# Kernel tuning notes

Hardware: AMD Instinct MI355X
Metric: run time of the kernel (lower is better)

The kernel has to match this reference:

```python
import jax, jax.numpy as jnp
import numpy as np

LN_EPS = 1e-5

def _gelu(x):
    # matches the module's custom gelu: x * sigmoid(1.702 * x)
    return x * jax.nn.sigmoid(1.702 * x)

def setup_inputs() -> dict:
    key = jax.random.key(0)
    k1, k2, k3, k4 = jax.random.split(key, 4)
    B, d_in, d_out, E = 4096, 768, 1024, 10
    x = jax.random.normal(k1, (B, d_in), dtype=jnp.float32)
    x_cls_logits = jax.random.normal(k2, (B, E), dtype=jnp.float32)
    # expert weights (torch Linear stored transposed; here [in, out] acting as x @ W)
    W1 = jax.random.normal(k3, (E, d_in, d_out), dtype=jnp.float32) * (d_in ** -0.5)
    W2 = jax.random.normal(k4, (E, d_out, d_out), dtype=jnp.float32) * (d_out ** -0.5)
    ln_gamma = jnp.ones((E, d_out), dtype=jnp.float32)
    ln_beta = jnp.zeros((E, d_out), dtype=jnp.float32)
    return {"x": x, "x_cls_logits": x_cls_logits, "W1": W1, "W2": W2,
            "ln_gamma": ln_gamma, "ln_beta": ln_beta}

def reference(x, x_cls_logits, W1, W2, ln_gamma, ln_beta):
    B = x.shape[0]
    # top-1 routing: each sample goes to expert argmax(x_cls)
    cls = jnp.argmax(x_cls_logits, axis=1)                       # [B] int
    # compute all experts densely, then select per sample (grouped equivalent of
    # the per-sample Python-loop dispatch in the original forward)
    embed1_all = jnp.einsum('bi,eio->beo', x, W1)                # [B,E,d_out]
    embed2_all = jnp.einsum('beo,eop->bep', _gelu(embed1_all), W2)  # [B,E,d_out]
    s_all = embed1_all + embed2_all                              # [B,E,d_out]
    rows = jnp.arange(B)
    s = s_all[rows, cls]                                         # [B,d_out]
    # per-expert LayerNorm params gathered per sample
    g = ln_gamma[cls]                                            # [B,d_out]
    b = ln_beta[cls]                                             # [B,d_out]
    mean = jnp.mean(s, axis=-1, keepdims=True)
    var = jnp.mean(jnp.square(s - mean), axis=-1, keepdims=True)
    y = (s - mean) * jax.lax.rsqrt(var + LN_EPS) * g + b
    # L2 normalize embeddings
    out = y / jnp.linalg.norm(y, axis=-1, keepdims=True)
    return out, x_cls_logits
```

## Files before the change

### kernel.cpp

```cpp
#include <hip/hip_runtime.h>
#include <math.h>

#define BSAMP 4096
#define D_IN  768
#define D_OUT 1024
#define NEXP  10
#define LN_EPS 1e-5f
#define STEPS1 (D_IN / 64)
#define STEPS2 (D_OUT / 64)

#define NB_CVT1 (D_IN / 32 * 4 * NEXP)
#define NB_CVT2 (D_OUT / 32 * 4 * NEXP)
#define NB_XCVT (BSAMP * D_IN / 2048)
#define NB_PREP (1 + NB_CVT1 + NB_CVT2 + NB_XCVT)

typedef __attribute__((ext_vector_type(8))) short bf16x8;
typedef __attribute__((ext_vector_type(4))) float f32x4;

__device__ __forceinline__ float b2f(unsigned short u) {
    union { unsigned int i; float f; } v; v.i = ((unsigned int)u) << 16; return v.f;
}
__device__ __forceinline__ unsigned short f2b(float f) {
    union { float f; unsigned int i; } v; v.f = f;
    unsigned int x = v.i;
    unsigned int r = (x + 0x7fffu + ((x >> 16) & 1u)) >> 16;
    return (unsigned short)r;
}


__device__ __forceinline__ void cvt_body(const float* __restrict__ W,
                                         unsigned short* __restrict__ Wt,
                                         int K, int i, int tid) {
    const int KT = K >> 5;
    const int kt = i % KT;
    const int rest = i / KT;
    const int n = (rest & 3) * 256 + tid;
    const int e = rest >> 2;
    const float* src = W + ((size_t)e * K + (size_t)kt * 32) * D_OUT + n;
    unsigned short v[32];
    #pragma unroll
    for (int j = 0; j < 32; j++) v[j] = f2b(src[(size_t)j * D_OUT]);
    const int nt = n >> 7, nn = n & 127;
    unsigned short* dst = Wt + ((((size_t)e * 8 + nt) * KT + kt) << 12) + nn * 32;
    #pragma unroll
    for (int j = 0; j < 4; j++)
        *(bf16x8*)&dst[j * 8] = *(bf16x8*)&v[j * 8];
}

__global__ __launch_bounds__(256)
void k7_prep(const float* __restrict__ logits, const float* __restrict__ X,
             const float* __restrict__ W1, const float* __restrict__ W2,
             float* __restrict__ out1, int* __restrict__ cls,
             int* __restrict__ idx, int* __restrict__ offs,
             unsigned short* __restrict__ xb, unsigned short* __restrict__ W1t,
             unsigned short* __restrict__ W2t) {
    const int tid = threadIdx.x;
    const int blk = blockIdx.x;

    if (blk == 0) {
        __shared__ int cnt[NEXP];
        __shared__ int cur[NEXP];
        __shared__ int offsL[NEXP + 1];
        if (tid < NEXP) cnt[tid] = 0;
        __syncthreads();

        int be[16];
        #pragma unroll
        for (int j = 0; j < 16; j++) {
            int b = tid + 256 * j;
            const float* L = logits + (size_t)b * NEXP;
            float best = L[0]; int e0 = 0;
            #pragma unroll
            for (int e = 0; e < NEXP; e++) {
                float v = L[e];
                out1[(size_t)b * NEXP + e] = v;
                if (v > best) { best = v; e0 = e; }
            }
            be[j] = e0;
            cls[b] = e0;
            atomicAdd(&cnt[e0], 1);
        }
        __syncthreads();
        if (tid == 0) {
            int s = 0;
            for (int e = 0; e < NEXP; e++) { offsL[e] = s; cur[e] = s; s += cnt[e]; }
            offsL[NEXP] = s;
        }
        __syncthreads();
        if (tid <= NEXP) offs[tid] = offsL[tid];
        #pragma unroll
        for (int j = 0; j < 16; j++) {
            int b = tid + 256 * j;
            int p = atomicAdd(&cur[be[j]], 1);
            idx[p] = b;
        }
        return;
    }

    int i = blk - 1;
    if (i < NB_CVT1) { cvt_body(W1, W1t, D_IN, i, tid); return; }
    i -= NB_CVT1;
    if (i < NB_CVT2) { cvt_body(W2, W2t, D_OUT, i, tid); return; }
    i -= NB_CVT2;
    {
        int o = (i * 256 + tid) * 8;
        float4 v0 = *(const float4*)(X + o);
        float4 v1 = *(const float4*)(X + o + 4);
        unsigned short t[8] = { f2b(v0.x), f2b(v0.y), f2b(v0.z), f2b(v0.w),
                                f2b(v1.x), f2b(v1.y), f2b(v1.z), f2b(v1.w) };
        *(bf16x8*)(xb + o) = *(bf16x8*)t;
    }
}


#define GLDS(srcp, dstp) __builtin_amdgcn_global_load_lds( \
    (const __attribute__((address_space(1))) unsigned int*)(srcp), \
    (__attribute__((address_space(3))) unsigned int*)(dstp), 16, 0, 0)

#define STAGE_A(Ab, t) do { \
    _Pragma("unroll") \
    for (int j = 0; j < 2; j++) { \
        int c = tid + j * 256; \
        GLDS(aRow + (t) * 64 + (c >> 6) * 8, (Ab) + c * 8); \
    } \
} while (0)

#define STAGE_B(Bb, t) do { \
    _Pragma("unroll") \
    for (int j = 0; j < 4; j++) { \
        int c = tid + j * 256; \
        int kc = c >> 7; \
        GLDS(bPanel + ((size_t)(2 * (t) + (kc >> 2)) << 12) + (c & 127) * 32 + (kc & 3) * 8, \
             (Bb) + c * 8); \
    } \
} while (0)

#define COMPUTE(Ab, Bb) do { \
    _Pragma("unroll") \
    for (int s = 0; s < 2; s++) { \
        const unsigned short* ab_ = (Ab) + (s * 4 + quad) * 512; \
        const unsigned short* bb_ = (Bb) + (s * 4 + quad) * 1024; \
        bf16x8 a0 = *(const bf16x8*)&ab_[(wrow + l16) * 8]; \
        bf16x8 a1 = *(const bf16x8*)&ab_[(wrow + 16 + l16) * 8]; \
        bf16x8 b0 = *(const bf16x8*)&bb_[(wcol + l16) * 8]; \
        bf16x8 b1 = *(const bf16x8*)&bb_[(wcol + 16 + l16) * 8]; \
        bf16x8 b2 = *(const bf16x8*)&bb_[(wcol + 32 + l16) * 8]; \
        bf16x8 b3 = *(const bf16x8*)&bb_[(wcol + 48 + l16) * 8]; \
        acc[0][0] = __builtin_amdgcn_mfma_f32_16x16x32_bf16(a0, b0, acc[0][0], 0, 0, 0); \
        acc[0][1] = __builtin_amdgcn_mfma_f32_16x16x32_bf16(a0, b1, acc[0][1], 0, 0, 0); \
        acc[0][2] = __builtin_amdgcn_mfma_f32_16x16x32_bf16(a0, b2, acc[0][2], 0, 0, 0); \
        acc[0][3] = __builtin_amdgcn_mfma_f32_16x16x32_bf16(a0, b3, acc[0][3], 0, 0, 0); \
        acc[1][0] = __builtin_amdgcn_mfma_f32_16x16x32_bf16(a1, b0, acc[1][0], 0, 0, 0); \
        acc[1][1] = __builtin_amdgcn_mfma_f32_16x16x32_bf16(a1, b1, acc[1][1], 0, 0, 0); \
        acc[1][2] = __builtin_amdgcn_mfma_f32_16x16x32_bf16(a1, b2, acc[1][2], 0, 0, 0); \
        acc[1][3] = __builtin_amdgcn_mfma_f32_16x16x32_bf16(a1, b3, acc[1][3], 0, 0, 0); \
    } \
} while (0)

__global__ __launch_bounds__(256)
void k6_gemm1(const unsigned short* __restrict__ xb, const unsigned short* __restrict__ W1t,
              const int* __restrict__ offs, const int* __restrict__ idx,
              unsigned short* __restrict__ e1g, unsigned short* __restrict__ g1g) {
    const int e = blockIdx.z;
    const int rowStart = offs[e] + blockIdx.y * 64;
    const int rowEnd = offs[e + 1];
    if (rowStart >= rowEnd) return;
    const int nt = blockIdx.x;

    __shared__ __align__(16) unsigned short A0[64 * 64], A1[64 * 64];
    __shared__ __align__(16) unsigned short B0[128 * 64], B1[128 * 64];
    __shared__ int rowIdxL[64];

    const int tid  = threadIdx.x;
    const int lane = tid & 63;
    const int wave = tid >> 6;
    const int quad = lane >> 4;
    const int l16  = lane & 15;
    const int wrow = (wave & 1) * 32;
    const int wcol = (wave >> 1) * 64;

    if (tid < 64) {
        int p = rowStart + tid;
        rowIdxL[tid] = idx[p < rowEnd ? p : rowEnd - 1];
    }
    __syncthreads();

    const unsigned short* aRow   = xb + (size_t)rowIdxL[tid & 63] * D_IN;
    const unsigned short* bPanel = W1t + ((((size_t)e * 8 + nt) * (D_IN / 32)) << 12);

    f32x4 acc[2][4];
    const f32x4 zf = {0.f, 0.f, 0.f, 0.f};
    #pragma unroll
    for (int r = 0; r < 2; r++)
        #pragma unroll
        for (int c = 0; c < 4; c++) acc[r][c] = zf;

    STAGE_A(A0, 0); STAGE_B(B0, 0);
    __syncthreads();
    for (int t = 0; t < STEPS1; t += 2) {
        STAGE_A(A1, t + 1); STAGE_B(B1, t + 1);
        COMPUTE(A0, B0);
        __syncthreads();
        if (t + 2 < STEPS1) { STAGE_A(A0, t + 2); STAGE_B(B0, t + 2); }
        COMPUTE(A1, B1);
        __syncthreads();
    }

    const int n0 = nt * 128;
    #pragma unroll
    for (int r = 0; r < 2; r++)
        #pragma unroll
        for (int q = 0; q < 4; q++) {
            int m = wrow + r * 16 + quad * 4 + q;
            int pp = rowStart + m;
            if (pp < rowEnd) {
                unsigned short* ep = e1g + (size_t)pp * D_OUT + n0 + wcol + l16;
                unsigned short* gp = g1g + (size_t)pp * D_OUT + n0 + wcol + l16;
                #pragma unroll
                for (int c = 0; c < 4; c++) {
                    unsigned short vb = f2b(acc[r][c][q]);
                    ep[c * 16] = vb;
                    float v = b2f(vb);
                    gp[c * 16] = f2b(v / (1.0f + __expf(-1.702f * v)));
                }
            }
        }
}

__global__ __launch_bounds__(256)
void k6_gemm2(const unsigned short* __restrict__ g1g, const unsigned short* __restrict__ e1g,
              const unsigned short* __restrict__ W2t,
              const int* __restrict__ offs, const int* __restrict__ idx,
              float* __restrict__ out0) {
    const int e = blockIdx.z;
    const int rowStart = offs[e] + blockIdx.y * 64;
    const int rowEnd = offs[e + 1];
    if (rowStart >= rowEnd) return;
    const int nt = blockIdx.x;

    __shared__ __align__(16) unsigned short A0[64 * 64], A1[64 * 64];
    __shared__ __align__(16) unsigned short B0[128 * 64], B1[128 * 64];
    __shared__ int rowIdxL[64];

    const int tid  = threadIdx.x;
    const int lane = tid & 63;
    const int wave = tid >> 6;
    const int quad = lane >> 4;
    const int l16  = lane & 15;
    const int wrow = (wave & 1) * 32;
    const int wcol = (wave >> 1) * 64;

    if (tid < 64) {
        int p = rowStart + tid;
        int ps = p < rowEnd ? p : rowEnd - 1;
        rowIdxL[tid] = idx[ps];
    }
    __syncthreads();

    int ap = rowStart + (tid & 63);
    const unsigned short* aRow   = g1g + (size_t)(ap < rowEnd ? ap : rowEnd - 1) * D_OUT;
    const unsigned short* bPanel = W2t + ((((size_t)e * 8 + nt) * (D_OUT / 32)) << 12);

    f32x4 acc[2][4];
    const f32x4 zf = {0.f, 0.f, 0.f, 0.f};
    #pragma unroll
    for (int r = 0; r < 2; r++)
        #pragma unroll
        for (int c = 0; c < 4; c++) acc[r][c] = zf;

    STAGE_A(A0, 0); STAGE_B(B0, 0);
    __syncthreads();
    for (int t = 0; t < STEPS2; t += 2) {
        STAGE_A(A1, t + 1); STAGE_B(B1, t + 1);
        COMPUTE(A0, B0);
        __syncthreads();
        if (t + 2 < STEPS2) { STAGE_A(A0, t + 2); STAGE_B(B0, t + 2); }
        COMPUTE(A1, B1);
        __syncthreads();
    }

    const int n0 = nt * 128;
    #pragma unroll
    for (int r = 0; r < 2; r++)
        #pragma unroll
        for (int q = 0; q < 4; q++) {
            int m = wrow + r * 16 + quad * 4 + q;
            int pp = rowStart + m;
            if (pp < rowEnd) {
                const unsigned short* ep = e1g + (size_t)pp * D_OUT + n0 + wcol + l16;
                float* op = out0 + (size_t)rowIdxL[m] * D_OUT + n0 + wcol + l16;
                #pragma unroll
                for (int c = 0; c < 4; c++)
                    op[c * 16] = acc[r][c][q] + b2f(ep[c * 16]);
            }
        }
}

__global__ __launch_bounds__(256)
void k4_ln(float* __restrict__ out0, const int* __restrict__ cls,
           const float* __restrict__ gam, const float* __restrict__ bet) {
    const int wave = threadIdx.x >> 6;
    const int lane = threadIdx.x & 63;
    const int b = blockIdx.x * 4 + wave;
    const int e = cls[b];

    float* row = out0 + (size_t)b * D_OUT + lane * 16;
    float v[16];
    #pragma unroll
    for (int j = 0; j < 4; j++) {
        float4 t = *(const float4*)(row + j * 4);
        v[j*4] = t.x; v[j*4+1] = t.y; v[j*4+2] = t.z; v[j*4+3] = t.w;
    }

    float sum = 0.f, sq = 0.f;
    #pragma unroll
    for (int j = 0; j < 16; j++) { sum += v[j]; sq += v[j] * v[j]; }
    #pragma unroll
    for (int o = 32; o; o >>= 1) { sum += __shfl_xor(sum, o, 64); sq += __shfl_xor(sq, o, 64); }
    float mean = sum * (1.0f / 1024.0f);
    float var = sq * (1.0f / 1024.0f) - mean * mean;
    float inv = rsqrtf(var + LN_EPS);

    const float* gp = gam + (size_t)e * D_OUT + lane * 16;
    const float* bp = bet + (size_t)e * D_OUT + lane * 16;
    float y[16]; float y2 = 0.f;
    #pragma unroll
    for (int j = 0; j < 16; j++) {
        y[j] = (v[j] - mean) * inv * gp[j] + bp[j];
        y2 += y[j] * y[j];
    }
    #pragma unroll
    for (int o = 32; o; o >>= 1) y2 += __shfl_xor(y2, o, 64);
    float rn = rsqrtf(y2);

    #pragma unroll
    for (int j = 0; j < 4; j++) {
        float4 t = { y[j*4] * rn, y[j*4+1] * rn, y[j*4+2] * rn, y[j*4+3] * rn };
        *(float4*)(row + j * 4) = t;
    }
}

extern "C" void kernel_launch(void* const* d_in, const int* in_sizes, int n_in,
                              void* d_out, int out_size, void* d_ws, size_t ws_size,
                              hipStream_t stream) {
    const float* x   = (const float*)d_in[0];
    const float* lg  = (const float*)d_in[1];
    const float* W1  = (const float*)d_in[2];
    const float* W2  = (const float*)d_in[3];
    const float* gam = (const float*)d_in[4];
    const float* bet = (const float*)d_in[5];
    float* out0 = (float*)d_out;
    float* out1 = out0 + (size_t)BSAMP * D_OUT;

    char* ws = (char*)d_ws;
    int* offs = (int*)ws;
    int* cls  = offs + 16;
    int* idx  = cls + BSAMP;
    unsigned short* W1t = (unsigned short*)(ws + 65536);
    unsigned short* W2t = W1t + (size_t)NEXP * D_IN * D_OUT;
    unsigned short* e1g = W2t + (size_t)NEXP * D_OUT * D_OUT;
    unsigned short* g1g = e1g + (size_t)BSAMP * D_OUT;
    unsigned short* xb  = g1g + (size_t)BSAMP * D_OUT;

    k7_prep<<<NB_PREP, 256, 0, stream>>>(lg, x, W1, W2, out1, cls, idx, offs,
                                         xb, W1t, W2t);

    dim3 g1(8, 64, NEXP);
    k6_gemm1<<<g1, 256, 0, stream>>>(xb, W1t, offs, idx, e1g, g1g);

    dim3 g2(8, 64, NEXP);
    k6_gemm2<<<g2, 256, 0, stream>>>(g1g, e1g, W2t, offs, idx, out0);

    k4_ln<<<BSAMP / 4, 256, 0, stream>>>(out0, cls, gam, bet);
}
```

Before: 209.8 us.

## Overlap W2 bf16 conversion with GEMM1 and vectorize weight conversion loads

Moves the W2 fp32-to-bf16 transpose conversion out of the prep kernel and appends it as extra blocks in the GEMM1 launch, so it can run concurrently with GEMM1 tiles (many of which exit early for underfilled experts). The weight conversion is also rewritten so each thread loads float4 along N and handles half of a 32-wide K slice, and X conversion processes 16 elements per thread. GEMM1 uses a flattened 1D grid. The cost is more work in the GEMM1 launch and a different store pattern for the converted weights.

```diff
diff --git a/kernel.cpp b/kernel.cpp
--- a/kernel.cpp
+++ b/kernel.cpp
@@ -9,10 +9,13 @@
 #define STEPS1 (D_IN / 64)
 #define STEPS2 (D_OUT / 64)
 
-#define NB_CVT1 (D_IN / 32 * 4 * NEXP)
-#define NB_CVT2 (D_OUT / 32 * 4 * NEXP)
-#define NB_XCVT (BSAMP * D_IN / 2048)
-#define NB_PREP (1 + NB_CVT1 + NB_CVT2 + NB_XCVT)
+#define NB_CVT1 (D_IN / 32 * 2 * NEXP)
+#define NB_XCVT (BSAMP * D_IN / (256 * 16))
+#define NB_PREP (1 + NB_CVT1 + NB_XCVT)
+
+#define NB_G1   (8 * 64 * NEXP)
+#define NB_CVT2 (D_OUT / 32 * 2 * NEXP)
+#define NB_G1ALL (NB_G1 + NB_CVT2)
 
 typedef __attribute__((ext_vector_type(8))) short bf16x8;
 typedef __attribute__((ext_vector_type(4))) float f32x4;
@@ -27,33 +30,33 @@
     return (unsigned short)r;
 }
 
-
-__device__ __forceinline__ void cvt_body(const float* __restrict__ W,
-                                         unsigned short* __restrict__ Wt,
-                                         int K, int i, int tid) {
+__device__ __forceinline__ void cvt16(const float* __restrict__ W,
+                                      unsigned short* __restrict__ Wt,
+                                      int K, int e, int kt, int kh, int tid) {
     const int KT = K >> 5;
-    const int kt = i % KT;
-    const int rest = i / KT;
-    const int n = (rest & 3) * 256 + tid;
-    const int e = rest >> 2;
-    const float* src = W + ((size_t)e * K + (size_t)kt * 32) * D_OUT + n;
-    unsigned short v[32];
-    #pragma unroll
-    for (int j = 0; j < 32; j++) v[j] = f2b(src[(size_t)j * D_OUT]);
+    const int n  = tid * 4;
+    const float* src = W + ((size_t)e * K + (size_t)kt * 32 + kh * 16) * D_OUT + n;
+    float4 v[16];
+    #pragma unroll
+    for (int j = 0; j < 16; j++) v[j] = *(const float4*)(src + (size_t)j * D_OUT);
     const int nt = n >> 7, nn = n & 127;
-    unsigned short* dst = Wt + ((((size_t)e * 8 + nt) * KT + kt) << 12) + nn * 32;
-    #pragma unroll
-    for (int j = 0; j < 4; j++)
-        *(bf16x8*)&dst[j * 8] = *(bf16x8*)&v[j * 8];
+    unsigned short* dst = Wt + ((((size_t)e * 8 + nt) * KT + kt) << 12) + nn * 32 + kh * 16;
+    #pragma unroll
+    for (int c = 0; c < 4; c++) {
+        unsigned short t[16];
+        #pragma unroll
+        for (int j = 0; j < 16; j++) t[j] = f2b(((const float*)&v[j])[c]);
+        *(bf16x8*)&dst[c * 32]     = *(bf16x8*)&t[0];
+        *(bf16x8*)&dst[c * 32 + 8] = *(bf16x8*)&t[8];
+    }
 }
 
 __global__ __launch_bounds__(256)
-void k7_prep(const float* __restrict__ logits, const float* __restrict__ X,
-             const float* __restrict__ W1, const float* __restrict__ W2,
+void k8_prep(const float* __restrict__ logits, const float* __restrict__ X,
+             const float* __restrict__ W1,
              float* __restrict__ out1, int* __restrict__ cls,
              int* __restrict__ idx, int* __restrict__ offs,
-             unsigned short* __restrict__ xb, unsigned short* __restrict__ W1t,
-             unsigned short* __restrict__ W2t) {
+             unsigned short* __restrict__ xb, unsigned short* __restrict__ W1t) {
     const int tid = threadIdx.x;
     const int blk = blockIdx.x;
 
@@ -98,17 +101,25 @@
     }
 
     int i = blk - 1;
-    if (i < NB_CVT1) { cvt_body(W1, W1t, D_IN, i, tid); return; }
+    if (i < NB_CVT1) {
+        int e = i / (D_IN / 32 * 2);
+        int r = i % (D_IN / 32 * 2);
+        cvt16(W1, W1t, D_IN, e, r >> 1, r & 1, tid);
+        return;
+    }
     i -= NB_CVT1;
-    if (i < NB_CVT2) { cvt_body(W2, W2t, D_OUT, i, tid); return; }
-    i -= NB_CVT2;
     {
-        int o = (i * 256 + tid) * 8;
+        int o = (i * 256 + tid) * 16;
         float4 v0 = *(const float4*)(X + o);
         float4 v1 = *(const float4*)(X + o + 4);
-        unsigned short t[8] = { f2b(v0.x), f2b(v0.y), f2b(v0.z), f2b(v0.w),
-                                f2b(v1.x), f2b(v1.y), f2b(v1.z), f2b(v1.w) };
-        *(bf16x8*)(xb + o) = *(bf16x8*)t;
+        float4 v2 = *(const float4*)(X + o + 8);
+        float4 v3 = *(const float4*)(X + o + 12);
+        unsigned short t[16] = { f2b(v0.x), f2b(v0.y), f2b(v0.z), f2b(v0.w),
+                                 f2b(v1.x), f2b(v1.y), f2b(v1.z), f2b(v1.w),
+                                 f2b(v2.x), f2b(v2.y), f2b(v2.z), f2b(v2.w),
+                                 f2b(v3.x), f2b(v3.y), f2b(v3.z), f2b(v3.w) };
+        *(bf16x8*)(xb + o)     = *(bf16x8*)&t[0];
+        *(bf16x8*)(xb + o + 8) = *(bf16x8*)&t[8];
     }
 }
 
@@ -158,20 +169,32 @@
 } while (0)
 
 __global__ __launch_bounds__(256)
-void k6_gemm1(const unsigned short* __restrict__ xb, const unsigned short* __restrict__ W1t,
+void k8_gemm1(const unsigned short* __restrict__ xb, const unsigned short* __restrict__ W1t,
+              const float* __restrict__ W2, unsigned short* __restrict__ W2t,
               const int* __restrict__ offs, const int* __restrict__ idx,
               unsigned short* __restrict__ e1g, unsigned short* __restrict__ g1g) {
-    const int e = blockIdx.z;
-    const int rowStart = offs[e] + blockIdx.y * 64;
+    const int tid = threadIdx.x;
+    const int blk = blockIdx.x;
+
+    if (blk >= NB_G1) {
+        int i = blk - NB_G1;
+        int e2 = i / (D_OUT / 32 * 2);
+        int r  = i % (D_OUT / 32 * 2);
+        cvt16(W2, W2t, D_OUT, e2, r >> 1, r & 1, tid);
+        return;
+    }
+
+    const int e  = blk >> 9;
+    const int rem = blk & 511;
+    const int rowStart = offs[e] + (rem >> 3) * 64;
     const int rowEnd = offs[e + 1];
     if (rowStart >= rowEnd) return;
-    const int nt = blockIdx.x;
+    const int nt = rem & 7;
 
     __shared__ __align__(16) unsigned short A0[64 * 64], A1[64 * 64];
     __shared__ __align__(16) unsigned short B0[128 * 64], B1[128 * 64];
     __shared__ int rowIdxL[64];
 
-    const int tid  = threadIdx.x;
     const int lane = tid & 63;
     const int wave = tid >> 6;
     const int quad = lane >> 4;
@@ -362,11 +385,9 @@
     unsigned short* g1g = e1g + (size_t)BSAMP * D_OUT;
     unsigned short* xb  = g1g + (size_t)BSAMP * D_OUT;
 
-    k7_prep<<<NB_PREP, 256, 0, stream>>>(lg, x, W1, W2, out1, cls, idx, offs,
-                                         xb, W1t, W2t);
-
-    dim3 g1(8, 64, NEXP);
-    k6_gemm1<<<g1, 256, 0, stream>>>(xb, W1t, offs, idx, e1g, g1g);
+    k8_prep<<<NB_PREP, 256, 0, stream>>>(lg, x, W1, out1, cls, idx, offs, xb, W1t);
+
+    k8_gemm1<<<NB_G1ALL, 256, 0, stream>>>(xb, W1t, W2, W2t, offs, idx, e1g, g1g);
 
     dim3 g2(8, 64, NEXP);
     k6_gemm2<<<g2, 256, 0, stream>>>(g1g, e1g, W2t, offs, idx, out0);
```

Result: slower. 214.5 us (+2.2%).
